# Kernel optimization log

Hardware: AMD Instinct MI355X
Metric: run time of the kernel (lower is better)

## Reference

```python
import jax, jax.numpy as jnp
import numpy as np

N_IN = 2048
N_OUT = 2048
RANK = 64
NUM_ITER = 4  # Newton-Schulz iterations, matches default num_iter=4


def setup_inputs() -> dict:
    key = jax.random.key(0)
    k1, k2, k3 = jax.random.split(key, 3)
    # scale U,V modestly so A = UV^T - VU^T is well-conditioned (mimics orthogonal init scale)
    scale = 1.0 / np.sqrt(N_IN)
    return {
        "input": jax.random.normal(k1, (8, 2048, N_IN), dtype=jnp.float32),
        "U": jax.random.normal(k2, (N_IN, RANK), dtype=jnp.float32) * scale,
        "V": jax.random.normal(k3, (N_IN, RANK), dtype=jnp.float32) * scale,
    }


def _orthogonal_weight(U, V):
    # A = U V^T - V U^T  (skew-symmetric, rank <= 2*rank)
    A = U @ V.T - V @ U.T              # [n, n]
    I = jnp.eye(N_IN, dtype=A.dtype)
    B = I - A
    X = I
    for _ in range(NUM_ITER):          # Newton-Schulz iteration for B^{-1}
        X = X @ (2.0 * I - B @ X)
    W_square = (I + A) @ X             # Cayley transform (I+A)(I-A)^{-1} approx
    return W_square[:N_OUT, :N_IN]


def reference(input, U, V):
    W = _orthogonal_weight(U, V)       # [out, in]
    # F.linear(input, W) = input @ W.T
    return jnp.einsum("bsi,oi->bso", input, W)
```

## Files before the change

### kernel.cpp

```cpp
#include <hip/hip_runtime.h>
#include <hip/hip_bf16.h>
#include <cstdint>
#include <cstddef>

#define NIN   2048
#define RANK  64
#define R2    128
#define NROWS 16384

typedef __bf16 bf16x8 __attribute__((ext_vector_type(8)));
typedef float  f32x4  __attribute__((ext_vector_type(4)));
typedef unsigned short u16x8 __attribute__((ext_vector_type(8)));

__device__ __forceinline__ unsigned short f2bf(float f) {
  union { float f; unsigned u; } x; x.f = f;
  return (unsigned short)((x.u + 0x7fffu + ((x.u >> 16) & 1u)) >> 16);
}

__global__ void k_prep(const float* __restrict__ U, const float* __restrict__ V,
                       unsigned short* __restrict__ Mf, float* __restrict__ G) {
  int b = blockIdx.x, tid = threadIdx.x;
  if (b < 128) {
    int CI = b * 256 + tid;
    int lane = CI & 63, J = (CI >> 6) & 63, t = CI >> 12;
    int n = t * 16 + (lane & 15);
    int k0 = J * 32 + (lane >> 4) * 8;
    const float* src = (n < RANK) ? (U + n) : (V + (n - RANK));
    u16x8 h;
#pragma unroll
    for (int e = 0; e < 8; ++e) h[e] = f2bf(src[(size_t)(k0 + e) * RANK]);
    *(u16x8*)(Mf + (size_t)CI * 8) = h;
  }
  int tile = b >> 3, ks = b & 7;
  int bi = tile >> 3, bj = tile & 7;
  int ty = tid >> 4, tx = tid & 15;
  int i = bi * 16 + ty, j = bj * 16 + tx;
  const float* Ai = (i < RANK) ? (U + i) : (V + (i - RANK));
  const float* Aj = (j < RANK) ? (U + j) : (V + (j - RANK));
  int k0 = ks * 256;
  float acc = 0.f;
#pragma unroll 8
  for (int k = k0; k < k0 + 256; ++k) acc += Ai[(size_t)k * RANK] * Aj[(size_t)k * RANK];
  if (i < RANK) atomicAdd(&G[(i + RANK) * R2 + j], -acc);
  else          atomicAdd(&G[(i - RANK) * R2 + j],  acc);
}

struct SOp { const float* A; const float* B; float* O; float a, b; };
struct SOps { SOp op[3]; };
__global__ void k_small(SOps ops) {
  SOp o = ops.op[blockIdx.x >> 6];
  int t = blockIdx.x & 63;
  int i = (t >> 3) * 16 + (threadIdx.x >> 4);
  int j = (t & 7) * 16 + (threadIdx.x & 15);
  float acc = 0.f;
#pragma unroll 8
  for (int k = 0; k < R2; ++k) {
    float av = o.A[i * R2 + k]; if (k == i) av += o.a;
    float bv = o.B[k * R2 + j]; if (k == j) bv += o.b;
    acc += av * bv;
  }
  o.O[i * R2 + j] = acc;
}

__global__ void k_D(const float* __restrict__ U, const float* __restrict__ V,
                    const float* __restrict__ H, const float* __restrict__ G15,
                    unsigned short* __restrict__ Df) {
  int idx = blockIdx.x * 256 + threadIdx.x;
  int i = idx >> 7, j = idx & 127;
  int jj = (j < RANK) ? (j + RANK) : (j - RANK);
  float sgn = (j < RANK) ? -1.f : 1.f;
  float acc = 0.f;
#pragma unroll 8
  for (int k = 0; k < R2; ++k) {
    float m = (k < RANK) ? U[(size_t)i * RANK + k] : V[(size_t)i * RANK + (k - RANK)];
    float t = 2.f * H[k * R2 + jj] - G15[k * R2 + jj];
    acc += m * (sgn * t);
  }
  int t_ = i >> 4, lr = i & 15;
  int J = j >> 5, lg = (j >> 3) & 3, e = j & 7;
  size_t CI = (size_t)(t_ * 4 + J) * 64 + lg * 16 + lr;
  Df[CI * 8 + e] = f2bf(acc);
}

__global__ __launch_bounds__(256) void k_T1(const float* __restrict__ input,
                                            const unsigned short* __restrict__ Mf,
                                            unsigned short* __restrict__ T1bf) {
  __shared__ __align__(16) unsigned char lds[73728];
  const int tid = threadIdx.x, lane = tid & 63, w = tid >> 6;
  const int lr = lane & 15, lg = lane >> 4;
  const int row0 = blockIdx.x * 32;
  unsigned char* abuf = lds + w * 8192;
  float* rbuf = (float*)lds;

  f32x4 acc[2][8] = {};
  const float* gbase = input + (size_t)row0 * NIN + w * 512;
  const int Jbase = w * 16;

  float4 s0[8], s1[8];
  bf16x8 bx[8], by[8];

#define T1_SLOAD(KT)                                                          \
  _Pragma("unroll") for (int p = 0; p < 8; ++p) {                             \
    int id = p * 64 + lane; int r = id >> 4, C = id & 15;                     \
    const float* g = gbase + (size_t)r * NIN + (KT) * 128 + C * 8;            \
    s0[p] = *(const float4*)g; s1[p] = *(const float4*)(g + 4);               \
  }
#define T1_SWRITE()                                                           \
  _Pragma("unroll") for (int p = 0; p < 8; ++p) {                             \
    int id = p * 64 + lane; int r = id >> 4, C = id & 15;                     \
    u16x8 h;                                                                  \
    h[0] = f2bf(s0[p].x); h[1] = f2bf(s0[p].y);                               \
    h[2] = f2bf(s0[p].z); h[3] = f2bf(s0[p].w);                               \
    h[4] = f2bf(s1[p].x); h[5] = f2bf(s1[p].y);                               \
    h[6] = f2bf(s1[p].z); h[7] = f2bf(s1[p].w);                               \
    *(u16x8*)(abuf + r * 256 + ((C ^ (r & 7)) << 4)) = h;                     \
  }
#define T1_BLOAD(P, S)                                                        \
  _Pragma("unroll") for (int t = 0; t < 8; ++t)                               \
    P[t] = *(const bf16x8*)(Mf + ((size_t)(t * 64 + Jbase + (S)) * 64 + lane) * 8);

  T1_SLOAD(0);
  T1_SWRITE();
  T1_BLOAD(bx, 0);

#pragma unroll
  for (int s = 0; s < 16; ++s) {
    const int kt = s >> 2, j = s & 3;
    if (j == 0 && kt < 3) { T1_SLOAD(kt + 1); }
    bf16x8 a0, a1;
    {
      int C = j * 4 + lg;
      a0 = *(const bf16x8*)(abuf + lr * 256 + ((C ^ (lr & 7)) << 4));
      a1 = *(const bf16x8*)(abuf + (16 + lr) * 256 + ((C ^ ((16 + lr) & 7)) << 4));
    }
    if (s < 15) { if (s & 1) { T1_BLOAD(bx, s + 1); } else { T1_BLOAD(by, s + 1); } }
#pragma unroll
    for (int t = 0; t < 8; ++t) {
      bf16x8 bcur = (s & 1) ? by[t] : bx[t];
      acc[0][t] = __builtin_amdgcn_mfma_f32_16x16x32_bf16(a0, bcur, acc[0][t], 0, 0, 0);
      acc[1][t] = __builtin_amdgcn_mfma_f32_16x16x32_bf16(a1, bcur, acc[1][t], 0, 0, 0);
    }
    if (j == 3 && kt < 3) { T1_SWRITE(); }
  }

  __syncthreads();
#pragma unroll
  for (int m = 0; m < 2; ++m)
#pragma unroll
    for (int t = 0; t < 8; ++t) {
      int col = t * 16 + lr, row = m * 16 + lg * 4;
      *(f32x4*)&rbuf[((size_t)w * 128 + col) * 36 + row] = acc[m][t];
    }
  __syncthreads();
  {
    int r = tid & 31, cg = tid >> 5;
    u16x8 o1, o2;
#pragma unroll
    for (int i = 0; i < 16; ++i) {
      int col = cg * 16 + i;
      float s = rbuf[(size_t)col * 36 + r]
              + rbuf[((size_t)128 + col) * 36 + r]
              + rbuf[((size_t)256 + col) * 36 + r]
              + rbuf[((size_t)384 + col) * 36 + r];
      if (i < 8) o1[i] = f2bf(s); else o2[i - 8] = f2bf(s);
    }
    unsigned short* dst = T1bf + (size_t)(row0 + r) * R2 + cg * 16;
    *(u16x8*)dst = o1;
    *(u16x8*)(dst + 8) = o2;
  }
}

__global__ __launch_bounds__(256) void k_OUT(const float* __restrict__ input,
                                             const unsigned short* __restrict__ T1bf,
                                             const unsigned short* __restrict__ Df,
                                             float* __restrict__ out) {
  __shared__ float obuf[4][32][132];
  const int tid = threadIdx.x, lane = tid & 63, w = tid >> 6;
  const int lr = lane & 15, lg = lane >> 4;
  const int row0 = blockIdx.x * 32;

  bf16x8 bq[2][4];
#pragma unroll
  for (int R = 0; R < 2; ++R)
#pragma unroll
    for (int J = 0; J < 4; ++J)
      bq[R][J] = *(const bf16x8*)(T1bf + (size_t)(row0 + R * 16 + lr) * R2 + J * 32 + lg * 8);

  bf16x8 xd[4], yd[4];
#define O_DLOAD(P, TTI)                                                       \
  _Pragma("unroll") for (int J = 0; J < 4; ++J)                               \
    P[J] = *(const bf16x8*)(Df + ((size_t)((w * 32 + (TTI)) * 4 + J) * 64 + lane) * 8);

  O_DLOAD(xd, 0);
#pragma unroll
  for (int g = 0; g < 4; ++g) {
#pragma unroll
    for (int tt = 0; tt < 8; ++tt) {
      const int tti = g * 8 + tt;
      if (tti < 31) { if (tti & 1) { O_DLOAD(xd, tti + 1); } else { O_DLOAD(yd, tti + 1); } }
#pragma unroll
      for (int R = 0; R < 2; ++R) {
        f32x4 o = {};
#pragma unroll
        for (int J = 0; J < 4; ++J) {
          bf16x8 d = (tti & 1) ? yd[J] : xd[J];
          o = __builtin_amdgcn_mfma_f32_16x16x32_bf16(d, bq[R][J], o, 0, 0, 0);
        }
        *(f32x4*)&obuf[w][R * 16 + lr][tt * 16 + lg * 4] = o;
      }
    }
#pragma unroll
    for (int c = 0; c < 16; ++c) {
      int id = c * 64 + lane;
      int r = id >> 5, cc = id & 31;
      f32x4 v = *(const f32x4*)&obuf[w][r][cc * 4];
      int grow = row0 + r, gcol = w * 512 + g * 128 + cc * 4;
      float4 inv = *(const float4*)(input + (size_t)grow * NIN + gcol);
      float4 res = { v[0] + inv.x, v[1] + inv.y, v[2] + inv.z, v[3] + inv.w };
      *(float4*)(out + (size_t)grow * NIN + gcol) = res;
    }
  }
}

extern "C" void kernel_launch(void* const* d_in, const int* in_sizes, int n_in,
                              void* d_out, int out_size, void* d_ws, size_t ws_size,
                              hipStream_t stream) {
  const float* input = (const float*)d_in[0];
  const float* U     = (const float*)d_in[1];
  const float* V     = (const float*)d_in[2];
  float* out = (float*)d_out;
  char* ws = (char*)d_ws;

  float* mats = (float*)ws;
  float* G   = mats + 0 * 16384;
  float* G2  = mats + 1 * 16384;
  float* G3  = mats + 2 * 16384;
  float* G4  = mats + 3 * 16384;
  float* G7  = mats + 4 * 16384;
  float* G8  = mats + 5 * 16384;
  float* H12 = mats + 6 * 16384;
  float* H124= mats + 7 * 16384;
  float* H   = mats + 8 * 16384;
  float* G15 = mats + 9 * 16384;
  unsigned short* Mf   = (unsigned short*)(ws + 10 * 65536);
  unsigned short* Df   = (unsigned short*)(ws + 10 * 65536 + 524288);
  unsigned short* T1bf = (unsigned short*)(ws + 10 * 65536 + 2 * 524288);

  hipMemsetAsync(G, 0, R2 * R2 * sizeof(float), stream);
  k_prep<<<512, 256, 0, stream>>>(U, V, Mf, G);
  k_T1<<<512, 256, 0, stream>>>(input, Mf, T1bf);

  { SOps o = {{ {G,  G,  G2, 0.f, 0.f}, {nullptr,nullptr,nullptr,0.f,0.f}, {nullptr,nullptr,nullptr,0.f,0.f} }};
    k_small<<<64, 256, 0, stream>>>(o); }
  { SOps o = {{ {G2, G2, G4, 0.f, 0.f}, {G2, G, G3, 0.f, 0.f}, {G, G2, H12, 1.f, 1.f} }};
    k_small<<<192, 256, 0, stream>>>(o); }
  { SOps o = {{ {G4, G4, G8, 0.f, 0.f}, {G3, G4, G7, 0.f, 0.f}, {H12, G4, H124, 0.f, 1.f} }};
    k_small<<<192, 256, 0, stream>>>(o); }
  { SOps o = {{ {G7, G8, G15, 0.f, 0.f}, {H124, G8, H, 0.f, 1.f}, {nullptr,nullptr,nullptr,0.f,0.f} }};
    k_small<<<128, 256, 0, stream>>>(o); }

  k_D<<<1024, 256, 0, stream>>>(U, V, H, G15, Df);
  k_OUT<<<512, 256, 0, stream>>>(input, T1bf, Df, out);
}
```

Before: 140.5 us.

## Fuse T1 projection and output kernels; drop atomics and memset in Gram prep

Merges the low-rank projection kernel and the output kernel into one, so each block keeps its 32x128 T1 tile in LDS instead of writing it to global memory and reading it back. The Gram matrix computation now gives each of 64 blocks the full K loop with plain stores, which removes the memset and the atomic adds. The projection step now runs after the small-matrix chain and D computation rather than overlapping them in stream order. The fused kernel also re-tiles the output staging into 64-column chunks so it fits the shared LDS footprint, at the cost of serial per-block work and a longer Gram prep loop.

```diff
diff --git a/kernel.cpp b/kernel.cpp
--- a/kernel.cpp
+++ b/kernel.cpp
@@ -30,19 +30,19 @@
 #pragma unroll
     for (int e = 0; e < 8; ++e) h[e] = f2bf(src[(size_t)(k0 + e) * RANK]);
     *(u16x8*)(Mf + (size_t)CI * 8) = h;
-  }
-  int tile = b >> 3, ks = b & 7;
-  int bi = tile >> 3, bj = tile & 7;
-  int ty = tid >> 4, tx = tid & 15;
-  int i = bi * 16 + ty, j = bj * 16 + tx;
-  const float* Ai = (i < RANK) ? (U + i) : (V + (i - RANK));
-  const float* Aj = (j < RANK) ? (U + j) : (V + (j - RANK));
-  int k0 = ks * 256;
-  float acc = 0.f;
+  } else {
+    int tile = b - 128;
+    int bi = tile >> 3, bj = tile & 7;
+    int ty = tid >> 4, tx = tid & 15;
+    int i = bi * 16 + ty, j = bj * 16 + tx;
+    const float* Ai = (i < RANK) ? (U + i) : (V + (i - RANK));
+    const float* Aj = (j < RANK) ? (U + j) : (V + (j - RANK));
+    float acc = 0.f;
 #pragma unroll 8
-  for (int k = k0; k < k0 + 256; ++k) acc += Ai[(size_t)k * RANK] * Aj[(size_t)k * RANK];
-  if (i < RANK) atomicAdd(&G[(i + RANK) * R2 + j], -acc);
-  else          atomicAdd(&G[(i - RANK) * R2 + j],  acc);
+    for (int k = 0; k < NIN; ++k) acc += Ai[(size_t)k * RANK] * Aj[(size_t)k * RANK];
+    if (i < RANK) G[(i + RANK) * R2 + j] = -acc;
+    else          G[(i - RANK) * R2 + j] =  acc;
+  }
 }
 
 struct SOp { const float* A; const float* B; float* O; float a, b; };
@@ -82,9 +82,10 @@
   Df[CI * 8 + e] = f2bf(acc);
 }
 
-__global__ __launch_bounds__(256) void k_T1(const float* __restrict__ input,
-                                            const unsigned short* __restrict__ Mf,
-                                            unsigned short* __restrict__ T1bf) {
+__global__ __launch_bounds__(256) void k_main(const float* __restrict__ input,
+                                              const unsigned short* __restrict__ Mf,
+                                              const unsigned short* __restrict__ Df,
+                                              float* __restrict__ out) {
   __shared__ __align__(16) unsigned char lds[73728];
   const int tid = threadIdx.x, lane = tid & 63, w = tid >> 6;
   const int lr = lane & 15, lg = lane >> 4;
@@ -95,7 +96,6 @@
   f32x4 acc[2][8] = {};
   const float* gbase = input + (size_t)row0 * NIN + w * 512;
   const int Jbase = w * 16;
-
   float4 s0[8], s1[8];
   bf16x8 bx[8], by[8];
 
@@ -122,7 +122,6 @@
   T1_SLOAD(0);
   T1_SWRITE();
   T1_BLOAD(bx, 0);
-
 #pragma unroll
   for (int s = 0; s < 16; ++s) {
     const int kt = s >> 2, j = s & 3;
@@ -154,38 +153,33 @@
   __syncthreads();
   {
     int r = tid & 31, cg = tid >> 5;
-    u16x8 o1, o2;
+    float sums[16];
 #pragma unroll
     for (int i = 0; i < 16; ++i) {
       int col = cg * 16 + i;
-      float s = rbuf[(size_t)col * 36 + r]
+      sums[i] = rbuf[(size_t)col * 36 + r]
               + rbuf[((size_t)128 + col) * 36 + r]
               + rbuf[((size_t)256 + col) * 36 + r]
               + rbuf[((size_t)384 + col) * 36 + r];
-      if (i < 8) o1[i] = f2bf(s); else o2[i - 8] = f2bf(s);
-    }
-    unsigned short* dst = T1bf + (size_t)(row0 + r) * R2 + cg * 16;
-    *(u16x8*)dst = o1;
-    *(u16x8*)(dst + 8) = o2;
-  }
-}
-
-__global__ __launch_bounds__(256) void k_OUT(const float* __restrict__ input,
-                                             const unsigned short* __restrict__ T1bf,
-                                             const unsigned short* __restrict__ Df,
-                                             float* __restrict__ out) {
-  __shared__ float obuf[4][32][132];
-  const int tid = threadIdx.x, lane = tid & 63, w = tid >> 6;
-  const int lr = lane & 15, lg = lane >> 4;
-  const int row0 = blockIdx.x * 32;
+    }
+    __syncthreads();
+    u16x8 o1, o2;
+#pragma unroll
+    for (int i = 0; i < 8; ++i) { o1[i] = f2bf(sums[i]); o2[i] = f2bf(sums[8 + i]); }
+    *(u16x8*)(lds + 65536 + r * 256 + (((cg * 2)     ^ (r & 7)) << 4)) = o1;
+    *(u16x8*)(lds + 65536 + r * 256 + (((cg * 2 + 1) ^ (r & 7)) << 4)) = o2;
+  }
+  __syncthreads();
 
   bf16x8 bq[2][4];
 #pragma unroll
   for (int R = 0; R < 2; ++R)
 #pragma unroll
-    for (int J = 0; J < 4; ++J)
-      bq[R][J] = *(const bf16x8*)(T1bf + (size_t)(row0 + R * 16 + lr) * R2 + J * 32 + lg * 8);
-
+    for (int J = 0; J < 4; ++J) {
+      int row = R * 16 + lr, cc = J * 4 + lg;
+      bq[R][J] = *(const bf16x8*)(lds + 65536 + row * 256 + ((cc ^ (row & 7)) << 4));
+    }
+  float* obufw = (float*)(lds + w * 8704);
   bf16x8 xd[4], yd[4];
 #define O_DLOAD(P, TTI)                                                       \
   _Pragma("unroll") for (int J = 0; J < 4; ++J)                               \
@@ -193,10 +187,10 @@
 
   O_DLOAD(xd, 0);
 #pragma unroll
-  for (int g = 0; g < 4; ++g) {
-#pragma unroll
-    for (int tt = 0; tt < 8; ++tt) {
-      const int tti = g * 8 + tt;
+  for (int g = 0; g < 8; ++g) {
+#pragma unroll
+    for (int tt = 0; tt < 4; ++tt) {
+      const int tti = g * 4 + tt;
       if (tti < 31) { if (tti & 1) { O_DLOAD(xd, tti + 1); } else { O_DLOAD(yd, tti + 1); } }
 #pragma unroll
       for (int R = 0; R < 2; ++R) {
@@ -206,15 +200,14 @@
           bf16x8 d = (tti & 1) ? yd[J] : xd[J];
           o = __builtin_amdgcn_mfma_f32_16x16x32_bf16(d, bq[R][J], o, 0, 0, 0);
         }
-        *(f32x4*)&obuf[w][R * 16 + lr][tt * 16 + lg * 4] = o;
+        *(f32x4*)&obufw[(R * 16 + lr) * 68 + tt * 16 + lg * 4] = o;
       }
     }
 #pragma unroll
-    for (int c = 0; c < 16; ++c) {
-      int id = c * 64 + lane;
-      int r = id >> 5, cc = id & 31;
-      f32x4 v = *(const f32x4*)&obuf[w][r][cc * 4];
-      int grow = row0 + r, gcol = w * 512 + g * 128 + cc * 4;
+    for (int c = 0; c < 8; ++c) {
+      int id = c * 64 + lane, r = id >> 4, cc = id & 15;
+      f32x4 v = *(const f32x4*)&obufw[r * 68 + cc * 4];
+      int grow = row0 + r, gcol = w * 512 + g * 64 + cc * 4;
       float4 inv = *(const float4*)(input + (size_t)grow * NIN + gcol);
       float4 res = { v[0] + inv.x, v[1] + inv.y, v[2] + inv.z, v[3] + inv.w };
       *(float4*)(out + (size_t)grow * NIN + gcol) = res;
@@ -242,13 +235,10 @@
   float* H124= mats + 7 * 16384;
   float* H   = mats + 8 * 16384;
   float* G15 = mats + 9 * 16384;
-  unsigned short* Mf   = (unsigned short*)(ws + 10 * 65536);
-  unsigned short* Df   = (unsigned short*)(ws + 10 * 65536 + 524288);
-  unsigned short* T1bf = (unsigned short*)(ws + 10 * 65536 + 2 * 524288);
-
-  hipMemsetAsync(G, 0, R2 * R2 * sizeof(float), stream);
-  k_prep<<<512, 256, 0, stream>>>(U, V, Mf, G);
-  k_T1<<<512, 256, 0, stream>>>(input, Mf, T1bf);
+  unsigned short* Mf = (unsigned short*)(ws + 10 * 65536);
+  unsigned short* Df = (unsigned short*)(ws + 10 * 65536 + 524288);
+
+  k_prep<<<192, 256, 0, stream>>>(U, V, Mf, G);
 
   { SOps o = {{ {G,  G,  G2, 0.f, 0.f}, {nullptr,nullptr,nullptr,0.f,0.f}, {nullptr,nullptr,nullptr,0.f,0.f} }};
     k_small<<<64, 256, 0, stream>>>(o); }
@@ -260,5 +250,5 @@
     k_small<<<128, 256, 0, stream>>>(o); }
 
   k_D<<<1024, 256, 0, stream>>>(U, V, H, G15, Df);
-  k_OUT<<<512, 256, 0, stream>>>(input, T1bf, Df, out);
-}
+  k_main<<<512, 256, 0, stream>>>(input, Mf, Df, out);
+}
```

After: 195.7 us. 1.39x slower.

## Fold G^2 small GEMM into T1 launch and drop memset/atomics in prep

Applied to the files above, without the earlier changes.

The memset of G goes away, and the atomic split-K reduction in k_prep is replaced by a 512-thread block that reduces two halves through shared memory and stores directly. The first small GEMM (G*G -> G2) moves into extra blocks of the k_T1 launch, which removes one kernel launch and lets it overlap with the large GEMM. This cuts launch count and serialization, but each G-tile block now has fewer parallel workers doing longer k-loops.

```diff
diff --git a/kernel.cpp b/kernel.cpp
--- a/kernel.cpp
+++ b/kernel.cpp
@@ -17,11 +17,30 @@
   return (unsigned short)((x.u + 0x7fffu + ((x.u >> 16) & 1u)) >> 16);
 }
 
-__global__ void k_prep(const float* __restrict__ U, const float* __restrict__ V,
-                       unsigned short* __restrict__ Mf, float* __restrict__ G) {
+__device__ __forceinline__ void smallGemm(const float* __restrict__ A,
+                                          const float* __restrict__ B,
+                                          float* __restrict__ O,
+                                          float a, float b, int t, int tid) {
+  int i = (t >> 3) * 16 + (tid >> 4);
+  int j = (t & 7) * 16 + (tid & 15);
+  float acc = 0.f;
+#pragma unroll 8
+  for (int k = 0; k < R2; ++k) {
+    float av = A[i * R2 + k]; if (k == i) av += a;
+    float bv = B[k * R2 + j]; if (k == j) bv += b;
+    acc += av * bv;
+  }
+  O[i * R2 + j] = acc;
+}
+
+__global__ __launch_bounds__(512) void k_prep(const float* __restrict__ U,
+                                              const float* __restrict__ V,
+                                              unsigned short* __restrict__ Mf,
+                                              float* __restrict__ G) {
+  __shared__ float red[512];
   int b = blockIdx.x, tid = threadIdx.x;
-  if (b < 128) {
-    int CI = b * 256 + tid;
+  if (b < 64) {
+    int CI = b * 512 + tid;
     int lane = CI & 63, J = (CI >> 6) & 63, t = CI >> 12;
     int n = t * 16 + (lane & 15);
     int k0 = J * 32 + (lane >> 4) * 8;
@@ -30,36 +49,33 @@
 #pragma unroll
     for (int e = 0; e < 8; ++e) h[e] = f2bf(src[(size_t)(k0 + e) * RANK]);
     *(u16x8*)(Mf + (size_t)CI * 8) = h;
-  }
-  int tile = b >> 3, ks = b & 7;
-  int bi = tile >> 3, bj = tile & 7;
-  int ty = tid >> 4, tx = tid & 15;
-  int i = bi * 16 + ty, j = bj * 16 + tx;
-  const float* Ai = (i < RANK) ? (U + i) : (V + (i - RANK));
-  const float* Aj = (j < RANK) ? (U + j) : (V + (j - RANK));
-  int k0 = ks * 256;
-  float acc = 0.f;
+  } else {
+    int tile = b - 64;
+    int bi = tile >> 3, bj = tile & 7;
+    int sub = tid >> 8, t256 = tid & 255;
+    int ty = t256 >> 4, tx = t256 & 15;
+    int i = bi * 16 + ty, j = bj * 16 + tx;
+    const float* Ai = (i < RANK) ? (U + i) : (V + (i - RANK));
+    const float* Aj = (j < RANK) ? (U + j) : (V + (j - RANK));
+    int k0 = sub * 1024;
+    float acc = 0.f;
 #pragma unroll 8
-  for (int k = k0; k < k0 + 256; ++k) acc += Ai[(size_t)k * RANK] * Aj[(size_t)k * RANK];
-  if (i < RANK) atomicAdd(&G[(i + RANK) * R2 + j], -acc);
-  else          atomicAdd(&G[(i - RANK) * R2 + j],  acc);
+    for (int k = k0; k < k0 + 1024; ++k) acc += Ai[(size_t)k * RANK] * Aj[(size_t)k * RANK];
+    red[tid] = acc;
+    __syncthreads();
+    if (sub == 0) {
+      float s = red[t256] + red[256 + t256];
+      if (i < RANK) G[(i + RANK) * R2 + j] = -s;
+      else          G[(i - RANK) * R2 + j] =  s;
+    }
+  }
 }
 
 struct SOp { const float* A; const float* B; float* O; float a, b; };
 struct SOps { SOp op[3]; };
 __global__ void k_small(SOps ops) {
   SOp o = ops.op[blockIdx.x >> 6];
-  int t = blockIdx.x & 63;
-  int i = (t >> 3) * 16 + (threadIdx.x >> 4);
-  int j = (t & 7) * 16 + (threadIdx.x & 15);
-  float acc = 0.f;
-#pragma unroll 8
-  for (int k = 0; k < R2; ++k) {
-    float av = o.A[i * R2 + k]; if (k == i) av += o.a;
-    float bv = o.B[k * R2 + j]; if (k == j) bv += o.b;
-    acc += av * bv;
-  }
-  o.O[i * R2 + j] = acc;
+  smallGemm(o.A, o.B, o.O, o.a, o.b, blockIdx.x & 63, threadIdx.x);
 }
 
 __global__ void k_D(const float* __restrict__ U, const float* __restrict__ V,
@@ -84,8 +100,14 @@
 
 __global__ __launch_bounds__(256) void k_T1(const float* __restrict__ input,
                                             const unsigned short* __restrict__ Mf,
-                                            unsigned short* __restrict__ T1bf) {
+                                            unsigned short* __restrict__ T1bf,
+                                            const float* __restrict__ G,
+                                            float* __restrict__ G2) {
   __shared__ __align__(16) unsigned char lds[73728];
+  if (blockIdx.x >= 512) {
+    smallGemm(G, G, G2, 0.f, 0.f, blockIdx.x - 512, threadIdx.x);
+    return;
+  }
   const int tid = threadIdx.x, lane = tid & 63, w = tid >> 6;
   const int lr = lane & 15, lg = lane >> 4;
   const int row0 = blockIdx.x * 32;
@@ -95,7 +117,6 @@
   f32x4 acc[2][8] = {};
   const float* gbase = input + (size_t)row0 * NIN + w * 512;
   const int Jbase = w * 16;
-
   float4 s0[8], s1[8];
   bf16x8 bx[8], by[8];
 
@@ -122,7 +143,6 @@
   T1_SLOAD(0);
   T1_SWRITE();
   T1_BLOAD(bx, 0);
-
 #pragma unroll
   for (int s = 0; s < 16; ++s) {
     const int kt = s >> 2, j = s & 3;
@@ -246,12 +266,9 @@
   unsigned short* Df   = (unsigned short*)(ws + 10 * 65536 + 524288);
   unsigned short* T1bf = (unsigned short*)(ws + 10 * 65536 + 2 * 524288);
 
-  hipMemsetAsync(G, 0, R2 * R2 * sizeof(float), stream);
-  k_prep<<<512, 256, 0, stream>>>(U, V, Mf, G);
-  k_T1<<<512, 256, 0, stream>>>(input, Mf, T1bf);
-
-  { SOps o = {{ {G,  G,  G2, 0.f, 0.f}, {nullptr,nullptr,nullptr,0.f,0.f}, {nullptr,nullptr,nullptr,0.f,0.f} }};
-    k_small<<<64, 256, 0, stream>>>(o); }
+  k_prep<<<128, 512, 0, stream>>>(U, V, Mf, G);
+  k_T1<<<576, 256, 0, stream>>>(input, Mf, T1bf, G, G2);
+
   { SOps o = {{ {G2, G2, G4, 0.f, 0.f}, {G2, G, G3, 0.f, 0.f}, {G, G2, H12, 1.f, 1.f} }};
     k_small<<<192, 256, 0, stream>>>(o); }
   { SOps o = {{ {G4, G4, G8, 0.f, 0.f}, {G3, G4, G7, 0.f, 0.f}, {H12, G4, H124, 0.f, 1.f} }};
```

After: 159.5 us. 1.14x slower.
